# Kernel tuning notes

Measured on AMD Instinct MI355X. Metric: run time of the kernel, lower is better.

Reference implementation:

```python
import jax, jax.numpy as jnp
import numpy as np

N, D, K = 131072, 64, 1024


def setup_inputs() -> dict:
    key = jax.random.key(0)
    kx, kc = jax.random.split(key)
    x = jax.random.normal(kx, (N, D), dtype=jnp.float32)
    # codebook ~ trunc_normal(std=0.2); plain normal*0.2 is a faithful stand-in
    codebook = 0.2 * jax.random.normal(kc, (K, D), dtype=jnp.float32)
    temperature = jnp.ones((1,), dtype=jnp.float32)
    return {"x": x, "codebook": codebook, "temperature": temperature}


def reference(x, codebook, temperature):
    # squared euclidean distances: [N, K]
    dist = (
        jnp.sum(x * x, axis=1, keepdims=True)
        + jnp.sum(codebook * codebook, axis=1)[None, :]
        - 2.0 * (x @ codebook.T)
    )
    neg_dist = -dist
    ids = jnp.argmax(neg_dist, axis=1)  # nearest code per row
    # Note: original tests `if self.train:` (a bound method, always truthy),
    # so the gumbel-softmax branch always executes.
    gkey = jax.random.key(42)
    g = jax.random.gumbel(gkey, neg_dist.shape, dtype=neg_dist.dtype)
    weights = jax.nn.softmax((neg_dist + g) / temperature[0], axis=-1)  # [N, K]
    emb = weights @ codebook  # [N, D]
    return emb, ids
```

## Files before the change

### kernel.cpp

```cpp
#include <hip/hip_runtime.h>
#include <stdint.h>

#define N_ROWS 131072
#define DIM 64
#define K_CODES 1024

typedef __attribute__((ext_vector_type(8))) short short8;
typedef __attribute__((ext_vector_type(4))) float float4v;
typedef __attribute__((ext_vector_type(4))) uint32_t u32x4;

#define LOG2E 1.4426950408889634f
#define LOG2_LN2 -0.5287663729448977f

#define TILE_B 13312

__device__ __forceinline__ uint32_t cvt_pk_bf16(float lo, float hi) {
    uint32_t r;
    asm("v_cvt_pk_bf16_f32 %0, %1, %2" : "=v"(r) : "v"(lo), "v"(hi));
    return r;
}
__device__ __forceinline__ uint32_t lo_pack(float fe, float fo, uint32_t h) {
    float le = fe - __uint_as_float(h << 16);
    float lo_ = fo - __uint_as_float(h & 0xffff0000u);
    return cvt_pk_bf16(le, lo_);
}
__device__ __forceinline__ float exp2_fast(float x) {
    float r; asm("v_exp_f32 %0, %1" : "=v"(r) : "v"(x)); return r;
}
__device__ __forceinline__ float log2_fast(float x) {
    float r; asm("v_log_f32 %0, %1" : "=v"(r) : "v"(x)); return r;
}

__device__ __forceinline__ void dma16(const void* g, void* l) {
    __builtin_amdgcn_global_load_lds(
        (const __attribute__((address_space(1))) uint32_t*)g,
        (__attribute__((address_space(3))) uint32_t*)l,
        16, 0, 0);
}

template<int V> struct IC { static constexpr int v = V; };

__global__ __launch_bounds__(256) void cbimg_kernel(const float* __restrict__ cb,
                                                    const float* __restrict__ temp,
                                                    uint16_t* __restrict__ img) {
    __shared__ float part[256];
    const int tile = blockIdx.x, tid = threadIdx.x;
    const int code = tid & 31, db = (tid >> 5) * 8;
    const int k = tile * 32 + code;
    const float invT = 1.0f / temp[0];
    const float sc = invT * LOG2E;
    const float4* src = reinterpret_cast<const float4*>(cb + (size_t)k * DIM + db);
    const float4 a = src[0], b = src[1];
    float ps = a.x*a.x;
    ps = fmaf(a.y, a.y, ps); ps = fmaf(a.z, a.z, ps); ps = fmaf(a.w, a.w, ps);
    ps = fmaf(b.x, b.x, ps); ps = fmaf(b.y, b.y, ps); ps = fmaf(b.z, b.z, ps);
    ps = fmaf(b.w, b.w, ps);
    part[(db >> 3) * 32 + code] = ps;
    uint32_t h0 = cvt_pk_bf16(a.x, a.y), h1 = cvt_pk_bf16(a.z, a.w);
    uint32_t h2 = cvt_pk_bf16(b.x, b.y), h3 = cvt_pk_bf16(b.z, b.w);
    const float sax = a.x*sc, say = a.y*sc, saz = a.z*sc, saw = a.w*sc;
    const float sbx = b.x*sc, sby = b.y*sc, sbz = b.z*sc, sbw = b.w*sc;
    uint32_t g0 = cvt_pk_bf16(sax, say), g1 = cvt_pk_bf16(saz, saw);
    uint32_t g2 = cvt_pk_bf16(sbx, sby), g3 = cvt_pk_bf16(sbz, sbw);
    u32x4 hv = {g0, g1, g2, g3};
    u32x4 lv = { lo_pack(sax,say,g0), lo_pack(saz,saw,g1),
                 lo_pack(sbx,sby,g2), lo_pack(sbz,sbw,g3) };
    uint16_t* t = img + (size_t)tile * (TILE_B / 2);
    *(u32x4*)&t[code*72 + db]        = hv;
    *(u32x4*)&t[2304 + code*72 + db] = lv;
    const int pc = ((code & 15) << 1) | (code >> 4);
    const uint16_t hh[8] = {
        (uint16_t)h0, (uint16_t)(h0 >> 16), (uint16_t)h1, (uint16_t)(h1 >> 16),
        (uint16_t)h2, (uint16_t)(h2 >> 16), (uint16_t)h3, (uint16_t)(h3 >> 16) };
    #pragma unroll
    for (int e = 0; e < 8; ++e) {
        const int row = db + e;
        t[4608 + row*32 + (((pc >> 3) ^ (row & 3)) << 3) + (pc & 7)] = hh[e];
    }
    __syncthreads();
    if (tid < 32) {
        float s = part[tid];
        #pragma unroll
        for (int i = 1; i < 8; ++i) s += part[i*32 + tid];
        *(float*)((char*)t + tid * 144 + 128) = fmaf(s, -sc, -LOG2_LN2);
    }
}

__device__ __forceinline__ uint32_t rotl32(uint32_t x, uint32_t r) {
    return __builtin_amdgcn_alignbit(x, x, 32u - r);
}
__device__ __forceinline__ void tf_round4(uint32_t x0[4], uint32_t x1[4], uint32_t r) {
    #pragma unroll
    for (int i = 0; i < 4; ++i) { x0[i] += x1[i]; x1[i] = rotl32(x1[i], r); x1[i] ^= x0[i]; }
}
__device__ __forceinline__ void threefry4w_k42(const uint32_t c0[4],
                                               uint32_t o0[4], uint32_t o1[4]) {
    const uint32_t ks1 = 42u, ks2 = 0x1BD11BDAu ^ 42u;
    uint32_t x0[4], x1[4];
    #pragma unroll
    for (int i = 0; i < 4; ++i) { x0[i] = c0[i]; x1[i] = c0[i] + (1u<<26) + ks1; }
    tf_round4(x0,x1,13); tf_round4(x0,x1,15); tf_round4(x0,x1,26); tf_round4(x0,x1,6);
    #pragma unroll
    for (int i = 0; i < 4; ++i) { x0[i] += ks1; x1[i] += ks2 + 1u; }
    tf_round4(x0,x1,17); tf_round4(x0,x1,29); tf_round4(x0,x1,16); tf_round4(x0,x1,24);
    #pragma unroll
    for (int i = 0; i < 4; ++i) { x0[i] += ks2; x1[i] += 2u; }
    tf_round4(x0,x1,13); tf_round4(x0,x1,15); tf_round4(x0,x1,26); tf_round4(x0,x1,6);
    #pragma unroll
    for (int i = 0; i < 4; ++i) { x1[i] += ks1 + 3u; }
    tf_round4(x0,x1,17); tf_round4(x0,x1,29); tf_round4(x0,x1,16); tf_round4(x0,x1,24);
    #pragma unroll
    for (int i = 0; i < 4; ++i) { x0[i] += ks1; x1[i] += ks2 + 4u; }
    tf_round4(x0,x1,13); tf_round4(x0,x1,15); tf_round4(x0,x1,26); tf_round4(x0,x1,6);
    #pragma unroll
    for (int i = 0; i < 4; ++i) { o0[i] = x0[i] + ks2; o1[i] = x1[i] + 5u; }
}

__device__ __forceinline__ float gumbel_l(uint32_t bits) {
    uint32_t fb = __builtin_amdgcn_alignbit(0x7Fu, bits, 9u);
    return log2_fast(__uint_as_float(fb) - 1.0f);
}

template<bool T1>
__device__ __forceinline__ void quant_body(
    const float* __restrict__ x, const uint16_t* __restrict__ img,
    const float* __restrict__ cb, const float invT,
    float* __restrict__ out_emb, float* __restrict__ out_ids, char* smem)
{
    uint16_t* const xhiP  = (uint16_t*)smem;
    uint16_t* const xloP  = (uint16_t*)(smem + 18432);
    uint16_t* const pbufP = (uint16_t*)(smem + 26624);

    const int tid  = threadIdx.x;
    const int wave = tid >> 6, lane = tid & 63, quad = lane >> 4, col = lane & 15;
    const int rowbase = blockIdx.x * 64 + wave * 8;

    {
        const int s = tid >> 2, w = s >> 4, t = s & 15, dq = tid & 3;
        const int row = blockIdx.x * 64 + w * 8 + (t >> 1) + ((t & 1) << 16);
        const float4* src = reinterpret_cast<const float4*>(x + (size_t)row * DIM + dq * 16);
        float4 f0 = src[0], f1 = src[1], f2 = src[2], f3 = src[3];
        u32x4 hA = { cvt_pk_bf16(f0.x,f0.y), cvt_pk_bf16(f0.z,f0.w),
                     cvt_pk_bf16(f1.x,f1.y), cvt_pk_bf16(f1.z,f1.w) };
        u32x4 hB = { cvt_pk_bf16(f2.x,f2.y), cvt_pk_bf16(f2.z,f2.w),
                     cvt_pk_bf16(f3.x,f3.y), cvt_pk_bf16(f3.z,f3.w) };
        u32x4 lA = { lo_pack(f0.x,f0.y,hA[0]), lo_pack(f0.z,f0.w,hA[1]),
                     lo_pack(f1.x,f1.y,hA[2]), lo_pack(f1.z,f1.w,hA[3]) };
        u32x4 lB = { lo_pack(f2.x,f2.y,hB[0]), lo_pack(f2.z,f2.w,hB[1]),
                     lo_pack(f3.x,f3.y,hB[2]), lo_pack(f3.z,f3.w,hB[3]) };
        uint16_t* dsth = &xhiP[(w*16 + t)*72 + dq*16];
        uint16_t* dstl = &xloP[(w*16 + t)*72 + dq*16];
        *(u32x4*)(dsth)     = hA;
        *(u32x4*)(dsth + 8) = hB;
        *(u32x4*)(dstl)     = lA;
        *(u32x4*)(dstl + 8) = lB;
    }
    __syncthreads();

    const int arb = (wave*16 + col)*72;
    const short8 ahi0 = *(const short8*)&xhiP[arb + quad*8];
    const short8 ahi1 = *(const short8*)&xhiP[arb + 32 + quad*8];
    const short8 alo0 = *(const short8*)&xloP[arb + quad*8];
    const short8 alo1 = *(const short8*)&xloP[arb + 32 + quad*8];
    __syncthreads();

    const char* gdma = (const char*)img + (size_t)lane * 16;
    auto dma_tile = [&](int tile, int bofs) {
        const char* s = gdma + (size_t)tile * TILE_B;
        char* d = smem + bofs;
        dma16(s + (size_t)wave*1024, d + wave*1024);
        if (wave < 5) dma16(s + (size_t)(wave+8)*1024, d + (wave+8)*1024);
    };
    dma_tile(0, 0);
    __syncthreads();

    const uint32_t base_c0 = (uint32_t)(rowbase + 2*quad) * 1024u + (uint32_t)col;

    float m[4]  = {-1e30f, -1e30f, -1e30f, -1e30f};
    float Zp[4] = {0.f, 0.f, 0.f, 0.f};
    float4v e0 = {0,0,0,0}, e1 = {0,0,0,0}, e2 = {0,0,0,0}, e3 = {0,0,0,0};
    float zt[4] = {-3.4e38f,-3.4e38f,-3.4e38f,-3.4e38f};
    float zs[4] = {-3.4e38f,-3.4e38f,-3.4e38f,-3.4e38f};
    int   kt[4] = {0,0,0,0}, ks[4] = {0,0,0,0};

    auto body = [&](int blk, auto B) {
        constexpr int BOF = decltype(B)::v;
        const uint16_t* cbhi = (const uint16_t*)(smem + BOF);
        const uint16_t* cblo = cbhi + 2304;
        const uint16_t* cbT  = cbhi + 4608;
        const int kb  = blk * 32;
        const int kc0 = kb + col, kc1 = kc0 + 16;

        if (blk + 1 < 32) dma_tile(blk + 1, BOF ^ TILE_B);
        const float nsc0 = *(const float*)&cbhi[col*72 + 64];
        const float nsc1 = *(const float*)&cbhi[(16 + col)*72 + 64];

        float l0c[4], l1c[4];
        {
            const uint32_t cA = base_c0 + (uint32_t)kb;
            const uint32_t c0s[4] = {cA, cA + 1024u, cA + 16u, cA + 1040u};
            uint32_t o0[4], o1[4];
            threefry4w_k42(c0s, o0, o1);
            float l[8];
            #pragma unroll
            for (int i = 0; i < 4; ++i) { l[2*i] = gumbel_l(o0[i]); l[2*i+1] = gumbel_l(o1[i]); }
            #pragma unroll
            for (int j = 0; j < 4; ++j) {
                if (T1) { l0c[j] = l[j]; l1c[j] = l[4+j]; }
                else {
                    l0c[j] = -invT * (log2_fast(-l[j])   + LOG2_LN2);
                    l1c[j] = -invT * (log2_fast(-l[4+j]) + LOG2_LN2);
                }
            }
        }

        float4v S0 = {0,0,0,0}, S1 = {0,0,0,0};
        {
            const int rb0 = col*72;
            const short8 bh0 = *(const short8*)&cbhi[rb0 + quad*8];
            const short8 bh1 = *(const short8*)&cbhi[rb0 + 32 + quad*8];
            const short8 bl0 = *(const short8*)&cblo[rb0 + quad*8];
            const short8 bl1 = *(const short8*)&cblo[rb0 + 32 + quad*8];
            S0 = __builtin_amdgcn_mfma_f32_16x16x32_bf16(ahi0, bh0, S0, 0,0,0);
            S0 = __builtin_amdgcn_mfma_f32_16x16x32_bf16(ahi1, bh1, S0, 0,0,0);
            S0 = __builtin_amdgcn_mfma_f32_16x16x32_bf16(ahi0, bl0, S0, 0,0,0);
            S0 = __builtin_amdgcn_mfma_f32_16x16x32_bf16(ahi1, bl1, S0, 0,0,0);
            S0 = __builtin_amdgcn_mfma_f32_16x16x32_bf16(alo0, bh0, S0, 0,0,0);
            S0 = __builtin_amdgcn_mfma_f32_16x16x32_bf16(alo1, bh1, S0, 0,0,0);
        }
        {
            const int rb1 = (16 + col)*72;
            const short8 bh0 = *(const short8*)&cbhi[rb1 + quad*8];
            const short8 bh1 = *(const short8*)&cbhi[rb1 + 32 + quad*8];
            const short8 bl0 = *(const short8*)&cblo[rb1 + quad*8];
            const short8 bl1 = *(const short8*)&cblo[rb1 + 32 + quad*8];
            S1 = __builtin_amdgcn_mfma_f32_16x16x32_bf16(ahi0, bh0, S1, 0,0,0);
            S1 = __builtin_amdgcn_mfma_f32_16x16x32_bf16(ahi1, bh1, S1, 0,0,0);
            S1 = __builtin_amdgcn_mfma_f32_16x16x32_bf16(ahi0, bl0, S1, 0,0,0);
            S1 = __builtin_amdgcn_mfma_f32_16x16x32_bf16(ahi1, bl1, S1, 0,0,0);
            S1 = __builtin_amdgcn_mfma_f32_16x16x32_bf16(alo0, bh0, S1, 0,0,0);
            S1 = __builtin_amdgcn_mfma_f32_16x16x32_bf16(alo1, bh1, S1, 0,0,0);
        }

        float z0v[4], z1v[4];
        #pragma unroll
        for (int j = 0; j < 4; ++j) {
            const float z0 = fmaf(S0[j], 2.0f, nsc0);
            const float z1 = fmaf(S1[j], 2.0f, nsc1);
            {   const bool c1 = z0 > zt[j], c2 = z0 > zs[j];
                const float zsn = __builtin_amdgcn_fmed3f(z0, zt[j], zs[j]);
                ks[j] = c1 ? kt[j] : (c2 ? kc0 : ks[j]);
                kt[j] = c1 ? kc0 : kt[j];
                zt[j] = fmaxf(zt[j], z0);
                zs[j] = zsn; }
            {   const bool c1 = z1 > zt[j], c2 = z1 > zs[j];
                const float zsn = __builtin_amdgcn_fmed3f(z1, zt[j], zs[j]);
                ks[j] = c1 ? kt[j] : (c2 ? kc1 : ks[j]);
                kt[j] = c1 ? kc1 : kt[j];
                zt[j] = fmaxf(zt[j], z1);
                zs[j] = zsn; }
            z0v[j] = z0; z1v[j] = z1;
        }

        if (T1) {
            #pragma unroll
            for (int j = 0; j < 4; ++j) {
                const float p0 = exp2_fast(z0v[j]) * __builtin_amdgcn_rcpf(-l0c[j]);
                const float p1 = exp2_fast(z1v[j]) * __builtin_amdgcn_rcpf(-l1c[j]);
                Zp[j] += p0 + p1;
                ((uint32_t*)pbufP)[(wave*16 + quad*4 + j)*20 + col] = cvt_pk_bf16(p0, p1);
            }
        } else {
            float a0[4], a1[4], zm[4];
            #pragma unroll
            for (int j = 0; j < 4; ++j) {
                a0[j] = z0v[j] + l0c[j];
                a1[j] = z1v[j] + l1c[j];
                zm[j] = fmaxf(a0[j], a1[j]);
            }
            float4v av;
            #pragma unroll
            for (int j = 0; j < 4; ++j) {
                float mn = fmaxf(m[j], zm[j]);
                #pragma unroll
                for (int mask = 1; mask < 16; mask <<= 1)
                    mn = fmaxf(mn, __shfl_xor(mn, mask));
                const float al = exp2_fast(m[j] - mn);
                m[j] = mn; Zp[j] *= al; av[j] = al;
            }
            e0 *= av; e1 *= av; e2 *= av; e3 *= av;
            #pragma unroll
            for (int j = 0; j < 4; ++j) {
                const float p0 = exp2_fast(a0[j] - m[j]);
                const float p1 = exp2_fast(a1[j] - m[j]);
                Zp[j] += p0 + p1;
                ((uint32_t*)pbufP)[(wave*16 + quad*4 + j)*20 + col] = cvt_pk_bf16(p0, p1);
            }
        }

        const short8 pa = *(const short8*)&pbufP[(wave*16 + col)*40 + quad*8];
        const int ts = (quad ^ (col & 3)) * 8;
        const short8 bt0 = *(const short8*)&cbT[( 0 + col)*32 + ts];
        const short8 bt1 = *(const short8*)&cbT[(16 + col)*32 + ts];
        const short8 bt2 = *(const short8*)&cbT[(32 + col)*32 + ts];
        const short8 bt3 = *(const short8*)&cbT[(48 + col)*32 + ts];
        e0 = __builtin_amdgcn_mfma_f32_16x16x32_bf16(pa, bt0, e0, 0,0,0);
        e1 = __builtin_amdgcn_mfma_f32_16x16x32_bf16(pa, bt1, e1, 0,0,0);
        e2 = __builtin_amdgcn_mfma_f32_16x16x32_bf16(pa, bt2, e2, 0,0,0);
        e3 = __builtin_amdgcn_mfma_f32_16x16x32_bf16(pa, bt3, e3, 0,0,0);

        __syncthreads();
    };

    for (int blk = 0; blk < 32; blk += 2) {
        body(blk,     IC<0>{});
        body(blk + 1, IC<TILE_B>{});
    }

    #pragma unroll
    for (int mask = 1; mask < 16; mask <<= 1) {
        #pragma unroll
        for (int j = 0; j < 4; ++j) Zp[j] += __shfl_xor(Zp[j], mask);
    }
    #pragma unroll
    for (int mask = 1; mask < 16; mask <<= 1) {
        #pragma unroll
        for (int j = 0; j < 4; ++j) {
            const float ozt = __shfl_xor(zt[j], mask);
            const float ozs = __shfl_xor(zs[j], mask);
            const int   okt = __shfl_xor(kt[j], mask);
            const int   oks = __shfl_xor(ks[j], mask);
            const bool mf = (zt[j] > ozt) || (zt[j] == ozt && kt[j] < okt);
            const float w1 = mf ? zt[j] : ozt;  const int wk1 = mf ? kt[j] : okt;
            const float l1 = mf ? ozt : zt[j];  const int lk1 = mf ? okt : kt[j];
            const float w2 = mf ? zs[j] : ozs;  const int wk2 = mf ? ks[j] : oks;
            const bool s1 = (l1 > w2) || (l1 == w2 && lk1 < wk2);
            zt[j] = w1; kt[j] = wk1;
            zs[j] = s1 ? l1 : w2; ks[j] = s1 ? lk1 : wk2;
        }
    }
    if (col == 0) {
        #pragma unroll
        for (int j = 0; j < 4; ++j) {
            if (zt[j] - zs[j] < 0.015f * invT) {
                const int t = quad*4 + j;
                const int row = rowbase + (t >> 1) + ((t & 1) << 16);
                const float* xr = x + (size_t)row * DIM;
                const float* cA = cb + (size_t)kt[j] * DIM;
                const float* cB = cb + (size_t)ks[j] * DIM;
                double dA = 0.0, dB = 0.0;
                for (int d = 0; d < DIM; ++d) {
                    const double xv = (double)xr[d];
                    const double av2 = (double)cA[d], bv = (double)cB[d];
                    dA = fma(av2, av2, dA); dA = fma(-2.0*xv, av2, dA);
                    dB = fma(bv,  bv,  dB); dB = fma(-2.0*xv, bv,  dB);
                }
                if (dB < dA || (dB == dA && ks[j] < kt[j])) kt[j] = ks[j];
            }
        }
    }
    #pragma unroll
    for (int j = 0; j < 4; ++j) {
        const int t = quad*4 + j;
        const int row = rowbase + (t >> 1) + ((t & 1) << 16);
        const float rZ = __builtin_amdgcn_rcpf(Zp[j]);
        out_emb[(size_t)row * DIM +      col] = e0[j] * rZ;
        out_emb[(size_t)row * DIM + 16 + col] = e1[j] * rZ;
        out_emb[(size_t)row * DIM + 32 + col] = e2[j] * rZ;
        out_emb[(size_t)row * DIM + 48 + col] = e3[j] * rZ;
        if (col == 0) out_ids[row] = (float)kt[j];
    }
}

__global__ __launch_bounds__(512) __attribute__((amdgpu_waves_per_eu(4, 4)))
void quant_kernel(
    const float* __restrict__ x, const uint16_t* __restrict__ img,
    const float* __restrict__ cb, const float* __restrict__ temp,
    float* __restrict__ out_emb, float* __restrict__ out_ids)
{
    __shared__ __align__(16) char smem[36864];
    const float invT = 1.0f / temp[0];
    if (invT == 1.0f) quant_body<true >(x, img, cb, invT, out_emb, out_ids, smem);
    else              quant_body<false>(x, img, cb, invT, out_emb, out_ids, smem);
}

extern "C" void kernel_launch(void* const* d_in, const int* in_sizes, int n_in,
                              void* d_out, int out_size, void* d_ws, size_t ws_size,
                              hipStream_t stream) {
    const float* x    = (const float*)d_in[0];
    const float* cb   = (const float*)d_in[1];
    const float* temp = (const float*)d_in[2];
    uint16_t* img     = (uint16_t*)d_ws;
    float* out_emb    = (float*)d_out;
    float* out_ids    = (float*)d_out + (size_t)N_ROWS * DIM;

    cbimg_kernel<<<32, 256, 0, stream>>>(cb, temp, img);
    quant_kernel<<<N_ROWS / 128, 512, 0, stream>>>(x, img, cb, temp, out_emb, out_ids);
}
```

Measured before the change: 298.6 us.

## Read codebook tiles directly from global memory instead of LDS double-buffering

Removes the global_load_lds double-buffered staging of the codebook image and has each wave read codebook fragments straight from global (L2/L1-cached) memory. The probability buffer becomes per-wave and reuses the x staging region, which removes all block-level barriers from the main loop. This saves the sync and DMA cost, but every wave now issues its own scattered global loads for shared codebook data, which adds latency and cache traffic. Because the x staging barrier is also dropped while pbuf aliases the x region, cross-wave read/write hazards are possible.

After: 339.5 us. 1.14x slower.

```diff
diff --git a/kernel.cpp b/kernel.cpp
--- a/kernel.cpp
+++ b/kernel.cpp
@@ -30,15 +30,6 @@
 __device__ __forceinline__ float log2_fast(float x) {
     float r; asm("v_log_f32 %0, %1" : "=v"(r) : "v"(x)); return r;
 }
-
-__device__ __forceinline__ void dma16(const void* g, void* l) {
-    __builtin_amdgcn_global_load_lds(
-        (const __attribute__((address_space(1))) uint32_t*)g,
-        (__attribute__((address_space(3))) uint32_t*)l,
-        16, 0, 0);
-}
-
-template<int V> struct IC { static constexpr int v = V; };
 
 __global__ __launch_bounds__(256) void cbimg_kernel(const float* __restrict__ cb,
                                                     const float* __restrict__ temp,
@@ -129,11 +120,11 @@
 {
     uint16_t* const xhiP  = (uint16_t*)smem;
     uint16_t* const xloP  = (uint16_t*)(smem + 18432);
-    uint16_t* const pbufP = (uint16_t*)(smem + 26624);
 
     const int tid  = threadIdx.x;
     const int wave = tid >> 6, lane = tid & 63, quad = lane >> 4, col = lane & 15;
     const int rowbase = blockIdx.x * 64 + wave * 8;
+    uint16_t* const pbufW = xhiP + wave * 1152;
 
     {
         const int s = tid >> 2, w = s >> 4, t = s & 15, dq = tid & 3;
@@ -155,24 +146,12 @@
         *(u32x4*)(dstl)     = lA;
         *(u32x4*)(dstl + 8) = lB;
     }
-    __syncthreads();
 
     const int arb = (wave*16 + col)*72;
     const short8 ahi0 = *(const short8*)&xhiP[arb + quad*8];
     const short8 ahi1 = *(const short8*)&xhiP[arb + 32 + quad*8];
     const short8 alo0 = *(const short8*)&xloP[arb + quad*8];
     const short8 alo1 = *(const short8*)&xloP[arb + 32 + quad*8];
-    __syncthreads();
-
-    const char* gdma = (const char*)img + (size_t)lane * 16;
-    auto dma_tile = [&](int tile, int bofs) {
-        const char* s = gdma + (size_t)tile * TILE_B;
-        char* d = smem + bofs;
-        dma16(s + (size_t)wave*1024, d + wave*1024);
-        if (wave < 5) dma16(s + (size_t)(wave+8)*1024, d + (wave+8)*1024);
-    };
-    dma_tile(0, 0);
-    __syncthreads();
 
     const uint32_t base_c0 = (uint32_t)(rowbase + 2*quad) * 1024u + (uint32_t)col;
 
@@ -183,15 +162,13 @@
     float zs[4] = {-3.4e38f,-3.4e38f,-3.4e38f,-3.4e38f};
     int   kt[4] = {0,0,0,0}, ks[4] = {0,0,0,0};
 
-    auto body = [&](int blk, auto B) {
-        constexpr int BOF = decltype(B)::v;
-        const uint16_t* cbhi = (const uint16_t*)(smem + BOF);
+    for (int blk = 0; blk < 32; ++blk) {
+        const uint16_t* cbhi = img + (size_t)blk * (TILE_B / 2);
         const uint16_t* cblo = cbhi + 2304;
         const uint16_t* cbT  = cbhi + 4608;
         const int kb  = blk * 32;
         const int kc0 = kb + col, kc1 = kc0 + 16;
 
-        if (blk + 1 < 32) dma_tile(blk + 1, BOF ^ TILE_B);
         const float nsc0 = *(const float*)&cbhi[col*72 + 64];
         const float nsc1 = *(const float*)&cbhi[(16 + col)*72 + 64];
 
@@ -268,7 +245,7 @@
                 const float p0 = exp2_fast(z0v[j]) * __builtin_amdgcn_rcpf(-l0c[j]);
                 const float p1 = exp2_fast(z1v[j]) * __builtin_amdgcn_rcpf(-l1c[j]);
                 Zp[j] += p0 + p1;
-                ((uint32_t*)pbufP)[(wave*16 + quad*4 + j)*20 + col] = cvt_pk_bf16(p0, p1);
+                ((uint32_t*)pbufW)[(quad*4 + j)*20 + col] = cvt_pk_bf16(p0, p1);
             }
         } else {
             float a0[4], a1[4], zm[4];
@@ -294,11 +271,11 @@
                 const float p0 = exp2_fast(a0[j] - m[j]);
                 const float p1 = exp2_fast(a1[j] - m[j]);
                 Zp[j] += p0 + p1;
-                ((uint32_t*)pbufP)[(wave*16 + quad*4 + j)*20 + col] = cvt_pk_bf16(p0, p1);
-            }
-        }
-
-        const short8 pa = *(const short8*)&pbufP[(wave*16 + col)*40 + quad*8];
+                ((uint32_t*)pbufW)[(quad*4 + j)*20 + col] = cvt_pk_bf16(p0, p1);
+            }
+        }
+
+        const short8 pa = *(const short8*)&pbufW[col*40 + quad*8];
         const int ts = (quad ^ (col & 3)) * 8;
         const short8 bt0 = *(const short8*)&cbT[( 0 + col)*32 + ts];
         const short8 bt1 = *(const short8*)&cbT[(16 + col)*32 + ts];
@@ -308,13 +285,6 @@
         e1 = __builtin_amdgcn_mfma_f32_16x16x32_bf16(pa, bt1, e1, 0,0,0);
         e2 = __builtin_amdgcn_mfma_f32_16x16x32_bf16(pa, bt2, e2, 0,0,0);
         e3 = __builtin_amdgcn_mfma_f32_16x16x32_bf16(pa, bt3, e3, 0,0,0);
-
-        __syncthreads();
-    };
-
-    for (int blk = 0; blk < 32; blk += 2) {
-        body(blk,     IC<0>{});
-        body(blk + 1, IC<TILE_B>{});
     }
 
     #pragma unroll
```
